# Performance work log

Hardware: AMD Instinct MI355X
Metric: run time of the kernel (lower is better)

Reference implementation:

```python
import jax, jax.numpy as jnp
import numpy as np

N = 50000        # nodes
E = 800000       # edges (pre self-loops)
H = 1            # heads
D = 64           # out_channels (incl. Lorentz time coord)
IN = 128         # in_channels
C = 1.0          # curvature c (Lorentz k)
EPS = 1e-6
NEG = 0.2        # leaky_relu negative slope


def segment_softmax(logits, seg, n):
    # numerically stable softmax over edges grouped by destination node
    m = jax.ops.segment_max(logits, seg, num_segments=n)
    m = jnp.where(jnp.isfinite(m), m, 0.0)
    e = jnp.exp(logits - m[seg])
    s = jax.ops.segment_sum(e, seg, num_segments=n)
    return e / (s[seg] + 1e-16)


def setup_inputs() -> dict:
    key = jax.random.key(0)
    k1, k2, k3, k4, k5 = jax.random.split(key, 5)
    x = jax.random.normal(k1, (N, IN), jnp.float32)
    fan = IN + H * (D - 1)
    W = jax.random.uniform(k2, (IN, H * (D - 1)), jnp.float32, -1.0, 1.0) * (6.0 / fan) ** 0.5
    b = jnp.zeros((H * (D - 1),), jnp.float32)
    att = jax.random.uniform(k3, (1, H, 2 * D), jnp.float32, -1.0, 1.0) * (6.0 / (H + 2 * D)) ** 0.5
    # random edges with no self loops (module removes them then re-adds canonical loops)
    src = jax.random.randint(k4, (E,), 0, N, jnp.int32)
    off = jax.random.randint(k5, (E,), 1, N, jnp.int32)
    dst = (src + off) % N
    edge_index = jnp.stack([src, dst], axis=0)
    return {"x": x, "W": W, "b": b, "att": att, "edge_index": edge_index}


def reference(x, W, b, att, edge_index):
    sqrt_c = C ** 0.5
    # add self loops
    loops = jnp.arange(N, dtype=edge_index.dtype)
    ei = jnp.concatenate([edge_index, jnp.stack([loops, loops])], axis=1)
    i, j = ei[0], ei[1]

    # hy_linear (plain Linear on Lorentz branch), then project to hyperboloid
    xs = (x @ W + b).reshape(N, H, D - 1)                       # space coords
    t = jnp.sqrt(jnp.sum(xs * xs, -1, keepdims=True) + C)       # time coord
    ox = jnp.concatenate([t, xs], -1)                           # (N,H,D) on manifold

    # Lorentz logmap0: d0 * (0, xs/||xs||), d0 = sqrt(c)*arccosh(x0/sqrt(c))
    nrm = jnp.sqrt(jnp.sum(xs * xs, -1, keepdims=True) + 1e-15)
    d0 = sqrt_c * jnp.arccosh(jnp.maximum(t / sqrt_c, 1.0 + EPS))
    log_x = jnp.concatenate([jnp.zeros_like(t), d0 * xs / nrm], -1)  # (N,H,D)

    x_i, x_j = log_x[i], log_x[j]        # (E2,H,D) edge gathers
    ox_i, ox_j = ox[i], ox[j]

    # attention logits
    alpha = jnp.sum(jnp.concatenate([x_i, x_j], -1) * att, -1)  # (E2,H)

    # distance-aware weighting: sqdist = c * arccosh(-<x,y>_L / c)^2
    inner = -ox_i[..., 0] * ox_j[..., 0] + jnp.sum(ox_i[..., 1:] * ox_j[..., 1:], -1)
    sqd = C * jnp.arccosh(jnp.maximum(-inner / C, 1.0 + EPS)) ** 2
    alpha = alpha * segment_softmax(sqd, i, N)

    alpha = jnp.where(alpha >= 0, alpha, NEG * alpha)           # leaky_relu
    alpha = segment_softmax(alpha, i, N)                        # (E2,H)

    out = jax.ops.segment_sum(alpha[..., None] * x_j, i, num_segments=N)  # (N,H,D)

    # proj_tan0 -> act -> proj_tan0
    out = out.at[..., 0].set(0.0)
    out = jax.nn.relu(out)
    out = out.at[..., 0].set(0.0)

    # expmap0 then projx
    usp = out[..., 1:]
    un = jnp.sqrt(jnp.sum(usp * usp, -1, keepdims=True) + 1e-15)
    sp = sqrt_c * jnp.sinh(un / sqrt_c) * usp / un
    time = jnp.sqrt(jnp.sum(sp * sp, -1, keepdims=True) + C)    # projx recomputes time
    y = jnp.concatenate([time, sp], -1)
    return y.reshape(N, H * D)
```

## Files before the change

### kernel.cpp

```cpp
#include <hip/hip_runtime.h>
#include <math.h>

#define NN 50000
#define EE 800000
#define ETOT 850000
#define INF 128
#define DD 64
#define CAP 64
#define NB_NODEBLK ((NN + 255) / 256)
#define NB_EDGE ((ETOT + 255) / 256)
#define KCH 16
#define XPITCH 265

__device__ __forceinline__ float wsum64(float v) {
#pragma unroll
    for (int m = 1; m < 64; m <<= 1) v += __shfl_xor(v, m, 64);
    return v;
}
__device__ __forceinline__ float rlf(float v, int k) {
    return __int_as_float(__builtin_amdgcn_readlane(__float_as_int(v), k));
}

__device__ __forceinline__ float mink_full(const float* __restrict__ ox,
                                           int j, float xnv) {
    const float4* ojp = (const float4*)(ox + (size_t)(unsigned)j * DD);
    float4 oj[16];
#pragma unroll
    for (int q = 0; q < 16; ++q) oj[q] = ojp[q];
    float p0 = 0.f, p1 = 0.f, p2 = 0.f, p3 = 0.f;
#pragma unroll
    for (int q = 0; q < 16; ++q) {
        p0 = fmaf(rlf(xnv, 4 * q + 0), oj[q].x, p0);
        p1 = fmaf(rlf(xnv, 4 * q + 1), oj[q].y, p1);
        p2 = fmaf(rlf(xnv, 4 * q + 2), oj[q].z, p2);
        p3 = fmaf(rlf(xnv, 4 * q + 3), oj[q].w, p3);
    }
    return (p0 + p1 + p2 + p3) - 2.f * rlf(xnv, 0) * oj[0].x;
}

__global__ __launch_bounds__(256) void k_node_place(
    const float* __restrict__ x, const float* __restrict__ W,
    const float* __restrict__ b, const float* __restrict__ att,
    const int* __restrict__ ei0, const int* __restrict__ ei1,
    float* __restrict__ ox, float* __restrict__ ai, float2* __restrict__ snd,
    int* __restrict__ cnt, int* __restrict__ colPad)
{
    __shared__ float Xl[KCH * XPITCH];

    if (blockIdx.x >= NB_NODEBLK) {
        int e = (blockIdx.x - NB_NODEBLK) * 256 + threadIdx.x;
        if (e < ETOT) {
            int i, j;
            if (e < EE) { i = ei0[e]; j = ei1[e]; }
            else        { i = e - EE; j = i; }
            int pos = atomicAdd(&cnt[i], 1);
            if (pos < CAP) colPad[(size_t)i * CAP + pos] = j;
        }
        return;
    }

    const int tid = threadIdx.x;
    const int n   = blockIdx.x * 256 + tid;

    float acc[63];
#pragma unroll
    for (int c = 0; c < 63; ++c) acc[c] = 0.f;

    const int nnq = tid >> 2;
    const int q   = tid & 3;

    for (int k0 = 0; k0 < INF; k0 += KCH) {
        __syncthreads();
#pragma unroll
        for (int r = 0; r < 4; ++r) {
            int nn = nnq + 64 * r;
            int gn = min(blockIdx.x * 256 + nn, NN - 1);
            float4 v = *(const float4*)(x + (size_t)gn * INF + k0 + 4 * q);
            Xl[(4 * q + 0) * XPITCH + nn] = v.x;
            Xl[(4 * q + 1) * XPITCH + nn] = v.y;
            Xl[(4 * q + 2) * XPITCH + nn] = v.z;
            Xl[(4 * q + 3) * XPITCH + nn] = v.w;
        }
        __syncthreads();
#pragma unroll
        for (int k = 0; k < KCH; ++k) {
            float xk = Xl[k * XPITCH + tid];
            const float* wr = W + (size_t)(k0 + k) * 63;
#pragma unroll
            for (int c = 0; c < 63; ++c)
                acc[c] = fmaf(xk, wr[c], acc[c]);
        }
    }

    if (n >= NN) return;

    float xs[63];
    float ss = 0.f;
#pragma unroll
    for (int c = 0; c < 63; ++c) {
        xs[c] = acc[c] + b[c];
        ss = fmaf(xs[c], xs[c], ss);
    }
    float t   = sqrtf(ss + 1.0f);
    float nrm = sqrtf(ss + 1e-15f);
    float d0  = acoshf(fmaxf(t, 1.0f + 1e-6f));
    float scl = d0 / nrm;

    float aiv = 0.f, ajv = 0.f;
#pragma unroll
    for (int c = 0; c < 63; ++c) {
        float lxv = scl * xs[c];
        aiv = fmaf(lxv, att[1 + c], aiv);
        ajv = fmaf(lxv, att[DD + 1 + c], ajv);
    }
    ai[n] = aiv;
    snd[n] = make_float2(ajv, scl);

    float4* orow = (float4*)(ox + (size_t)n * DD);
    orow[0] = make_float4(t, xs[0], xs[1], xs[2]);
#pragma unroll
    for (int g = 1; g < 16; ++g)
        orow[g] = make_float4(xs[4 * g - 1], xs[4 * g], xs[4 * g + 1], xs[4 * g + 2]);
}

__global__ __launch_bounds__(256) void k_fused(
    const int* __restrict__ cnt, const int* __restrict__ colPad,
    const float* __restrict__ ox, const float* __restrict__ ai,
    const float2* __restrict__ snd, float* __restrict__ y)
{
    const int lane = threadIdx.x & 63;
    const int wid  = threadIdx.x >> 6;
    const int n = blockIdx.x * 4 + wid;
    if (n >= NN) return;

    const int base = n * CAP;
    int deg = cnt[n];
    if (deg > CAP) deg = CAP;
    const float aii = ai[n];
    const float xnv = ox[(size_t)n * DD + lane];

    const bool act = lane < deg;
    const int  ecl = min(lane, deg - 1);
    const int  jreg = colPad[base + ecl];
    const float2 sv = snd[jreg];

    float inner = mink_full(ox, jreg, xnv);
    float arg = fmaxf(-inner, 1.0f + 1e-6f);
    float dd0 = acoshf(arg);
    float sq  = dd0 * dd0;

    float e1 = act ? expf(sq) : 0.f;
    float s1 = wsum64(e1) + 1e-16f;
    float al = (aii + sv.x) * e1 / s1;
    al = (al >= 0.f) ? al : 0.2f * al;
    float p2 = act ? expf(al) : 0.f;
    float s2 = wsum64(p2);
    float w2 = p2 / (s2 + 1e-16f) * sv.y;

    float acc = 0.f;
    int k = 0;
    for (; k + 8 <= deg; k += 8) {
        float w0 = __shfl(w2, k + 0, 64), w1 = __shfl(w2, k + 1, 64);
        float w2b = __shfl(w2, k + 2, 64), w3 = __shfl(w2, k + 3, 64);
        float w4 = __shfl(w2, k + 4, 64), w5 = __shfl(w2, k + 5, 64);
        float w6 = __shfl(w2, k + 6, 64), w7 = __shfl(w2, k + 7, 64);
        int j0 = __shfl(jreg, k + 0, 64), j1 = __shfl(jreg, k + 1, 64);
        int j2 = __shfl(jreg, k + 2, 64), j3 = __shfl(jreg, k + 3, 64);
        int j4 = __shfl(jreg, k + 4, 64), j5 = __shfl(jreg, k + 5, 64);
        int j6 = __shfl(jreg, k + 6, 64), j7 = __shfl(jreg, k + 7, 64);
        float v0 = ox[(size_t)j0 * DD + lane], v1 = ox[(size_t)j1 * DD + lane];
        float v2 = ox[(size_t)j2 * DD + lane], v3 = ox[(size_t)j3 * DD + lane];
        float v4 = ox[(size_t)j4 * DD + lane], v5 = ox[(size_t)j5 * DD + lane];
        float v6 = ox[(size_t)j6 * DD + lane], v7 = ox[(size_t)j7 * DD + lane];
        acc = fmaf(w0, v0, acc);  acc = fmaf(w1, v1, acc);
        acc = fmaf(w2b, v2, acc); acc = fmaf(w3, v3, acc);
        acc = fmaf(w4, v4, acc);  acc = fmaf(w5, v5, acc);
        acc = fmaf(w6, v6, acc);  acc = fmaf(w7, v7, acc);
    }
    for (; k < deg; ++k) {
        float w = __shfl(w2, k, 64);
        int   j = __shfl(jreg, k, 64);
        acc = fmaf(w, ox[(size_t)j * DD + lane], acc);
    }

    float usp = (lane == 0) ? 0.f : fmaxf(acc, 0.f);
    float ss = wsum64(usp * usp);
    float un = sqrtf(ss + 1e-15f);
    float sc = sinhf(un) / un;
    float sp = sc * usp;
    float time = sqrtf(sc * sc * ss + 1.0f);
    y[(size_t)n * DD + lane] = (lane == 0) ? time : sp;
}

extern "C" void kernel_launch(void* const* d_in, const int* in_sizes, int n_in,
                              void* d_out, int out_size, void* d_ws, size_t ws_size,
                              hipStream_t stream) {
    const float* x   = (const float*)d_in[0];
    const float* W   = (const float*)d_in[1];
    const float* b   = (const float*)d_in[2];
    const float* att = (const float*)d_in[3];
    const int*   ei  = (const int*)d_in[4];
    const int* ei0 = ei;
    const int* ei1 = ei + EE;
    float* out = (float*)d_out;

    float*  ws  = (float*)d_ws;
    float*  ox  = ws;
    float*  ai  = ox + (size_t)NN * DD;
    float2* snd = (float2*)(ai + NN);
    int*    cnt    = (int*)(snd + NN);
    int*    colPad = cnt + NN;

    hipMemsetAsync(cnt, 0, sizeof(int) * NN, stream);

    k_node_place<<<NB_NODEBLK + NB_EDGE, 256, 0, stream>>>(
        x, W, b, att, ei0, ei1, ox, ai, snd, cnt, colPad);

    k_fused<<<(NN + 3) / 4, 256, 0, stream>>>(cnt, colPad, ox, ai, snd, out);
}
```

Baseline: 146.8 us.

## Split node transform across two half-blocks and separate edge placement kernel

The node linear-transform kernel now gives each node to two threads, each holding half of the 63 output columns. Partial norms and attention dots are combined through shared memory. This cuts per-thread register use and doubles the block count, aiming for higher occupancy. The edge-placement work moves into its own kernel launched before the node kernel, which adds a launch and removes the overlap the combined grid had.

```diff
diff --git a/kernel.cpp b/kernel.cpp
--- a/kernel.cpp
+++ b/kernel.cpp
@@ -7,10 +7,10 @@
 #define INF 128
 #define DD 64
 #define CAP 64
-#define NB_NODEBLK ((NN + 255) / 256)
+#define NB_NODEBLK ((NN + 127) / 128)
 #define NB_EDGE ((ETOT + 255) / 256)
-#define KCH 16
-#define XPITCH 265
+#define KCH 32
+#define XP 132
 
 __device__ __forceinline__ float wsum64(float v) {
 #pragma unroll
@@ -38,89 +38,132 @@
     return (p0 + p1 + p2 + p3) - 2.f * rlf(xnv, 0) * oj[0].x;
 }
 
-__global__ __launch_bounds__(256) void k_node_place(
+__global__ __launch_bounds__(256, 4) void k_node(
     const float* __restrict__ x, const float* __restrict__ W,
     const float* __restrict__ b, const float* __restrict__ att,
-    const int* __restrict__ ei0, const int* __restrict__ ei1,
-    float* __restrict__ ox, float* __restrict__ ai, float2* __restrict__ snd,
-    int* __restrict__ cnt, int* __restrict__ colPad)
+    float* __restrict__ ox, float* __restrict__ ai, float2* __restrict__ snd)
 {
-    __shared__ float Xl[KCH * XPITCH];
-
-    if (blockIdx.x >= NB_NODEBLK) {
-        int e = (blockIdx.x - NB_NODEBLK) * 256 + threadIdx.x;
-        if (e < ETOT) {
-            int i, j;
-            if (e < EE) { i = ei0[e]; j = ei1[e]; }
-            else        { i = e - EE; j = i; }
-            int pos = atomicAdd(&cnt[i], 1);
-            if (pos < CAP) colPad[(size_t)i * CAP + pos] = j;
-        }
-        return;
-    }
+    __shared__ float Xl[KCH * XP];
+    __shared__ float pp0[256], pp1[256], pp2[256];
 
     const int tid = threadIdx.x;
-    const int n   = blockIdx.x * 256 + tid;
-
-    float acc[63];
-#pragma unroll
-    for (int c = 0; c < 63; ++c) acc[c] = 0.f;
-
-    const int nnq = tid >> 2;
-    const int q   = tid & 3;
+    const int h   = tid >> 7;
+    const int ns  = tid & 127;
+    const int n   = blockIdx.x * 128 + ns;
+    const bool valid = n < NN;
+    const int NC = h ? 32 : 31;
+
+    float acc[32];
+#pragma unroll
+    for (int c = 0; c < 32; ++c) acc[c] = 0.f;
 
     for (int k0 = 0; k0 < INF; k0 += KCH) {
         __syncthreads();
 #pragma unroll
         for (int r = 0; r < 4; ++r) {
-            int nn = nnq + 64 * r;
-            int gn = min(blockIdx.x * 256 + nn, NN - 1);
+            int idx = r * 256 + tid;
+            int nd = idx >> 3, q = idx & 7;
+            int gn = min(blockIdx.x * 128 + nd, NN - 1);
             float4 v = *(const float4*)(x + (size_t)gn * INF + k0 + 4 * q);
-            Xl[(4 * q + 0) * XPITCH + nn] = v.x;
-            Xl[(4 * q + 1) * XPITCH + nn] = v.y;
-            Xl[(4 * q + 2) * XPITCH + nn] = v.z;
-            Xl[(4 * q + 3) * XPITCH + nn] = v.w;
+            Xl[(4 * q + 0) * XP + nd] = v.x;
+            Xl[(4 * q + 1) * XP + nd] = v.y;
+            Xl[(4 * q + 2) * XP + nd] = v.z;
+            Xl[(4 * q + 3) * XP + nd] = v.w;
         }
         __syncthreads();
-#pragma unroll
-        for (int k = 0; k < KCH; ++k) {
-            float xk = Xl[k * XPITCH + tid];
-            const float* wr = W + (size_t)(k0 + k) * 63;
-#pragma unroll
-            for (int c = 0; c < 63; ++c)
-                acc[c] = fmaf(xk, wr[c], acc[c]);
-        }
-    }
-
-    if (n >= NN) return;
-
-    float xs[63];
-    float ss = 0.f;
-#pragma unroll
-    for (int c = 0; c < 63; ++c) {
-        xs[c] = acc[c] + b[c];
-        ss = fmaf(xs[c], xs[c], ss);
-    }
+        if (h == 0) {
+#pragma unroll
+            for (int k = 0; k < KCH; ++k) {
+                float xk = Xl[k * XP + ns];
+                const float* wr = W + (size_t)(k0 + k) * 63;
+#pragma unroll
+                for (int c = 0; c < 31; ++c)
+                    acc[c] = fmaf(xk, wr[c], acc[c]);
+            }
+        } else {
+#pragma unroll
+            for (int k = 0; k < KCH; ++k) {
+                float xk = Xl[k * XP + ns];
+                const float* wr = W + (size_t)(k0 + k) * 63 + 31;
+#pragma unroll
+                for (int c = 0; c < 32; ++c)
+                    acc[c] = fmaf(xk, wr[c], acc[c]);
+            }
+        }
+    }
+
+    float ssp = 0.f;
+    if (h == 0) {
+#pragma unroll
+        for (int c = 0; c < 31; ++c) {
+            acc[c] += b[c];
+            ssp = fmaf(acc[c], acc[c], ssp);
+        }
+    } else {
+#pragma unroll
+        for (int c = 0; c < 32; ++c) {
+            acc[c] += b[31 + c];
+            ssp = fmaf(acc[c], acc[c], ssp);
+        }
+    }
+    pp0[tid] = ssp;
+    __syncthreads();
+    float ss = ssp + pp0[tid ^ 128];
+
     float t   = sqrtf(ss + 1.0f);
     float nrm = sqrtf(ss + 1e-15f);
     float d0  = acoshf(fmaxf(t, 1.0f + 1e-6f));
     float scl = d0 / nrm;
 
     float aiv = 0.f, ajv = 0.f;
-#pragma unroll
-    for (int c = 0; c < 63; ++c) {
-        float lxv = scl * xs[c];
-        aiv = fmaf(lxv, att[1 + c], aiv);
-        ajv = fmaf(lxv, att[DD + 1 + c], ajv);
-    }
-    ai[n] = aiv;
-    snd[n] = make_float2(ajv, scl);
-
-    float4* orow = (float4*)(ox + (size_t)n * DD);
-    orow[0] = make_float4(t, xs[0], xs[1], xs[2]);
-#pragma unroll
-    for (int g = 1; g < 16; ++g)
-        orow[g] = make_float4(xs[4 * g - 1], xs[4 * g], xs[4 * g + 1], xs[4 * g + 2]);
+    if (h == 0) {
+#pragma unroll
+        for (int c = 0; c < 31; ++c) {
+            float lxv = scl * acc[c];
+            aiv = fmaf(lxv, att[1 + c], aiv);
+            ajv = fmaf(lxv, att[DD + 1 + c], ajv);
+        }
+    } else {
+#pragma unroll
+        for (int c = 0; c < 32; ++c) {
+            float lxv = scl * acc[c];
+            aiv = fmaf(lxv, att[1 + 31 + c], aiv);
+            ajv = fmaf(lxv, att[DD + 1 + 31 + c], ajv);
+        }
+    }
+    pp1[tid] = aiv; pp2[tid] = ajv;
+    __syncthreads();
+
+    if (valid) {
+        float4* orow = (float4*)(ox + (size_t)n * DD);
+        if (h == 0) {
+            ai[n]  = aiv + pp1[tid ^ 128];
+            snd[n] = make_float2(ajv + pp2[tid ^ 128], scl);
+            orow[0] = make_float4(t, acc[0], acc[1], acc[2]);
+#pragma unroll
+            for (int g = 1; g < 8; ++g)
+                orow[g] = make_float4(acc[4 * g - 1], acc[4 * g],
+                                      acc[4 * g + 1], acc[4 * g + 2]);
+        } else {
+#pragma unroll
+            for (int g = 0; g < 8; ++g)
+                orow[8 + g] = make_float4(acc[4 * g], acc[4 * g + 1],
+                                          acc[4 * g + 2], acc[4 * g + 3]);
+        }
+    }
+}
+
+__global__ __launch_bounds__(256) void k_place(
+    const int* __restrict__ ei0, const int* __restrict__ ei1,
+    int* __restrict__ cnt, int* __restrict__ colPad)
+{
+    int e = blockIdx.x * 256 + threadIdx.x;
+    if (e >= ETOT) return;
+    int i, j;
+    if (e < EE) { i = ei0[e]; j = ei1[e]; }
+    else        { i = e - EE; j = i; }
+    int pos = atomicAdd(&cnt[i], 1);
+    if (pos < CAP) colPad[(size_t)i * CAP + pos] = j;
 }
 
 __global__ __launch_bounds__(256) void k_fused(
@@ -213,8 +256,7 @@
 
     hipMemsetAsync(cnt, 0, sizeof(int) * NN, stream);
 
-    k_node_place<<<NB_NODEBLK + NB_EDGE, 256, 0, stream>>>(
-        x, W, b, att, ei0, ei1, ox, ai, snd, cnt, colPad);
-
+    k_place<<<NB_EDGE, 256, 0, stream>>>(ei0, ei1, cnt, colPad);
+    k_node<<<NB_NODEBLK, 256, 0, stream>>>(x, W, b, att, ox, ai, snd);
     k_fused<<<(NN + 3) / 4, 256, 0, stream>>>(cnt, colPad, ox, ai, snd, out);
 }
```

After: 195.9 us. 1.34x slower.
